# Kernel tuning notes

Hardware: AMD Instinct MI355X
Metric: run time of the kernel (lower is better)

## Reference

```python
import jax, jax.numpy as jnp
import numpy as np

B, T, D, H = 4, 2048, 1024, 16
HS = D // H  # 64
SCALE = float(HS) ** (-5)  # faithful to source: head_size ** (-5), NOT -0.5
EPS = 1e-5


def layer_norm(x, g, b):
    m = jnp.mean(x, axis=-1, keepdims=True)
    v = jnp.mean(jnp.square(x - m), axis=-1, keepdims=True)
    return (x - m) * jax.lax.rsqrt(v + EPS) * g + b


def setup_inputs() -> dict:
    key = jax.random.key(0)
    ks = jax.random.split(key, 8)
    s = 0.02
    return {
        "x": jax.random.normal(ks[0], (B, T, D), dtype=jnp.float32),
        "Wk": jax.random.normal(ks[1], (H, D, HS), dtype=jnp.float32) * s,  # shared by q (source bug: q = self.key(x))
        "Wv": jax.random.normal(ks[2], (H, D, HS), dtype=jnp.float32) * s,
        "Wo": jax.random.normal(ks[3], (H * HS, D), dtype=jnp.float32) * s,
        "bo": jnp.zeros((D,), dtype=jnp.float32),
        "g1": jnp.ones((D,), dtype=jnp.float32),
        "b1": jnp.zeros((D,), dtype=jnp.float32),
        "Wf1": jax.random.normal(ks[4], (D, D), dtype=jnp.float32) * s,
        "bf1": jnp.zeros((D,), dtype=jnp.float32),
        "Wf2": jax.random.normal(ks[5], (D, D), dtype=jnp.float32) * s,
        "bf2": jnp.zeros((D,), dtype=jnp.float32),
        "g2": jnp.ones((D,), dtype=jnp.float32),
        "b2": jnp.zeros((D,), dtype=jnp.float32),
    }


def reference(x, Wk, Wv, Wo, bo, g1, b1, Wf1, bf1, Wf2, bf2, g2, b2):
    # per-head projections; source uses key weights for BOTH q and k, so q == k
    k = jnp.einsum('btd,hds->bhts', x, Wk)           # [B,H,T,HS]
    v = jnp.einsum('btd,hds->bhts', x, Wv)           # [B,H,T,HS]
    wei = jnp.einsum('bhts,bhus->bhtu', k, k) * SCALE  # q==k; [B,H,T,T]
    causal = jnp.tril(jnp.ones((T, T), dtype=bool))
    wei = jnp.where(causal, wei, -jnp.inf)
    wei = jax.nn.softmax(wei, axis=-1)
    attn = jnp.einsum('bhtu,bhus->bhts', wei, v)     # [B,H,T,HS]
    cat = attn.transpose(0, 2, 1, 3).reshape(B, T, H * HS)  # concat heads
    attn_out = cat @ Wo + bo                         # output projection
    norm = layer_norm(attn_out + x, g1, b1)
    ff = jax.nn.relu(norm @ Wf1 + bf1) @ Wf2 + bf2
    return layer_norm(ff + norm + x, g2, b2)
```

## Files before the change

### kernel.cpp

```cpp
#include <hip/hip_runtime.h>

typedef unsigned short u16;
typedef __attribute__((ext_vector_type(8))) short short8;
typedef __attribute__((ext_vector_type(4))) float f32x4;

constexpr int Bn = 4, Tn = 2048, Dn = 1024, Hn = 16, HSn = 64;
constexpr long BT = (long)Bn * Tn;
#define NSEG 64
#define SEG (Tn / NSEG)

__device__ __forceinline__ u16 f2bf(float f) {
    union { float f; unsigned u; } x; x.f = f;
    unsigned r = x.u + 0x7FFFu + ((x.u >> 16) & 1u);
    return (u16)(r >> 16);
}
__device__ __forceinline__ float bf2f(unsigned bits16) {
    union { unsigned u; float f; } x; x.u = bits16 << 16;
    return x.f;
}

__device__ __forceinline__ void async_load16(const u16* g, u16* lds) {
    __builtin_amdgcn_global_load_lds(
        (const __attribute__((address_space(1))) unsigned*)g,
        (__attribute__((address_space(3))) unsigned*)lds, 16, 0, 0);
}

__global__ __launch_bounds__(256) void prep_kernel(
    const float* __restrict__ x, const float* __restrict__ Wv,
    const float* __restrict__ Wo, const float* __restrict__ Wf1,
    const float* __restrict__ Wf2,
    u16* __restrict__ xb, u16* __restrict__ WvC,
    u16* __restrict__ WoT, u16* __restrict__ Wf1T, u16* __restrict__ Wf2T)
{
    __shared__ float tile[32][33];
    const int blk = blockIdx.x;
    if (blk < 8192) {
        long i = (long)blk * 256 + threadIdx.x;
        float4 v = ((const float4*)x)[i];
        unsigned lo = (unsigned)f2bf(v.x) | ((unsigned)f2bf(v.y) << 16);
        unsigned hi = (unsigned)f2bf(v.z) | ((unsigned)f2bf(v.w) << 16);
        ((uint2*)xb)[i] = make_uint2(lo, hi);
    } else if (blk < 12288) {
        long i = (long)(blk - 8192) * 256 + threadIdx.x;
        int d = (int)(i >> 10), c = (int)(i & 1023);
        int h = c >> 6, s = c & 63;
        WvC[i] = f2bf(Wv[((long)h * Dn + d) * HSn + s]);
    } else {
        int idx = blk - 12288;
        int z = idx >> 10, rem = idx & 1023;
        const float* in = z == 0 ? Wo : (z == 1 ? Wf1 : Wf2);
        u16* out        = z == 0 ? WoT : (z == 1 ? Wf1T : Wf2T);
        int k0 = (rem & 31) * 32, n0 = (rem >> 5) * 32;
        int tx = threadIdx.x & 31, ty = threadIdx.x >> 5;
        #pragma unroll
        for (int r = 0; r < 4; r++)
            tile[ty + r * 8][tx] = in[(long)(k0 + ty + r * 8) * Dn + n0 + tx];
        __syncthreads();
        #pragma unroll
        for (int r = 0; r < 4; r++)
            out[(long)(n0 + ty + r * 8) * Dn + k0 + tx] = f2bf(tile[tx][ty + r * 8]);
    }
}

__global__ __launch_bounds__(256) void mfma_gemm(
    const u16* __restrict__ A,
    const u16* __restrict__ BT,
    float* __restrict__ Cf,
    u16* __restrict__ Cb,
    const float* __restrict__ bias, int relu, int K, int N,
    float* __restrict__ segs_out)
{
    __shared__ __attribute__((aligned(16))) u16 As[128 * 64];
    __shared__ __attribute__((aligned(16))) u16 Bs[128 * 64];

    const int t = threadIdx.x;
    const int wv = t >> 6, ln = t & 63;
    const int lane15 = ln & 15, q = ln >> 4;
    const int row0 = blockIdx.x * 128, n0 = blockIdx.y * 128;
    const int mq = (wv >> 1) * 64, nq = (wv & 1) * 64;

    f32x4 acc[4][4];
    #pragma unroll
    for (int i = 0; i < 4; i++)
        #pragma unroll
        for (int j = 0; j < 4; j++)
            acc[i][j] = (f32x4){0.f, 0.f, 0.f, 0.f};

    for (int k0 = 0; k0 < K; k0 += 64) {
        #pragma unroll
        for (int jj = 0; jj < 4; jj++) {
            int Ibase = wv * 256 + jj * 64;
            int I = Ibase + ln;
            int m = I >> 3, pc = I & 7, c = pc ^ (m & 7);
            async_load16(&A[(long)(row0 + m) * K + k0 + c * 8], &As[Ibase * 8]);
        }
        #pragma unroll
        for (int jj = 0; jj < 4; jj++) {
            int Ibase = wv * 256 + jj * 64;
            int I = Ibase + ln;
            int m = I >> 3, pc = I & 7, c = pc ^ (m & 7);
            async_load16(&BT[(long)(n0 + m) * K + k0 + c * 8], &Bs[Ibase * 8]);
        }
        __syncthreads();

        #pragma unroll
        for (int kk = 0; kk < 2; kk++) {
            short8 af[4], bfr[4];
            #pragma unroll
            for (int i = 0; i < 4; i++) {
                int mr = mq + i * 16 + lane15;
                int ca = (kk * 4 + q) ^ (mr & 7);
                af[i] = *(const short8*)&As[(mr * 8 + ca) * 8];
                int nr = nq + i * 16 + lane15;
                int cb = (kk * 4 + q) ^ (nr & 7);
                bfr[i] = *(const short8*)&Bs[(nr * 8 + cb) * 8];
            }
            #pragma unroll
            for (int i = 0; i < 4; i++)
                #pragma unroll
                for (int j = 0; j < 4; j++)
                    acc[i][j] = __builtin_amdgcn_mfma_f32_16x16x32_bf16(
                        af[i], bfr[j], acc[i][j], 0, 0, 0);
        }
        __syncthreads();
    }

    if (segs_out) {
        int segbase = (row0 + mq) >> 5;
        #pragma unroll
        for (int j = 0; j < 4; j++) {
            float s01 = 0.f, s23 = 0.f;
            #pragma unroll
            for (int r = 0; r < 4; r++) {
                s01 += acc[0][j][r] + acc[1][j][r];
                s23 += acc[2][j][r] + acc[3][j][r];
            }
            s01 += __shfl_xor(s01, 16); s01 += __shfl_xor(s01, 32);
            s23 += __shfl_xor(s23, 16); s23 += __shfl_xor(s23, 32);
            int col = n0 + nq + j * 16 + lane15;
            if (q == 0) segs_out[(long)segbase * Dn + col] = s01;
            if (q == 1) segs_out[(long)(segbase + 1) * Dn + col] = s23;
        }
    }

    #pragma unroll
    for (int j = 0; j < 4; j++) {
        int col = n0 + nq + j * 16 + lane15;
        float bv = bias ? bias[col] : 0.f;
        #pragma unroll
        for (int i = 0; i < 4; i++) {
            #pragma unroll
            for (int r = 0; r < 4; r++) {
                long row = row0 + mq + i * 16 + q * 4 + r;
                float v = acc[i][j][r] + bv;
                if (relu) v = fmaxf(v, 0.f);
                if (Cf) Cf[row * N + col] = v;
                if (Cb) Cb[row * N + col] = f2bf(v);
            }
        }
    }
}

__global__ __launch_bounds__(256) void mfma_gemm64(
    const u16* __restrict__ A, const u16* __restrict__ BT,
    u16* __restrict__ Cb, int K, int N)
{
    __shared__ __attribute__((aligned(16))) u16 As[64 * 64];
    __shared__ __attribute__((aligned(16))) u16 Bs[64 * 64];

    const int t = threadIdx.x;
    const int wv = t >> 6, ln = t & 63;
    const int lane15 = ln & 15, q = ln >> 4;
    const int row0 = blockIdx.x * 64, n0 = blockIdx.y * 64;
    const int mq = (wv >> 1) * 32, nq = (wv & 1) * 32;

    f32x4 acc[2][2];
    #pragma unroll
    for (int i = 0; i < 2; i++)
        #pragma unroll
        for (int j = 0; j < 2; j++)
            acc[i][j] = (f32x4){0.f, 0.f, 0.f, 0.f};

    for (int k0 = 0; k0 < K; k0 += 64) {
        #pragma unroll
        for (int jj = 0; jj < 2; jj++) {
            int Ibase = wv * 128 + jj * 64;
            int I = Ibase + ln;
            int m = I >> 3, pc = I & 7, c = pc ^ (m & 7);
            async_load16(&A[(long)(row0 + m) * K + k0 + c * 8], &As[Ibase * 8]);
        }
        #pragma unroll
        for (int jj = 0; jj < 2; jj++) {
            int Ibase = wv * 128 + jj * 64;
            int I = Ibase + ln;
            int m = I >> 3, pc = I & 7, c = pc ^ (m & 7);
            async_load16(&BT[(long)(n0 + m) * K + k0 + c * 8], &Bs[Ibase * 8]);
        }
        __syncthreads();

        #pragma unroll
        for (int kk = 0; kk < 2; kk++) {
            short8 af[2], bfr[2];
            #pragma unroll
            for (int i = 0; i < 2; i++) {
                int mr = mq + i * 16 + lane15;
                int ca = (kk * 4 + q) ^ (mr & 7);
                af[i] = *(const short8*)&As[(mr * 8 + ca) * 8];
                int nr = nq + i * 16 + lane15;
                int cb = (kk * 4 + q) ^ (nr & 7);
                bfr[i] = *(const short8*)&Bs[(nr * 8 + cb) * 8];
            }
            #pragma unroll
            for (int i = 0; i < 2; i++)
                #pragma unroll
                for (int j = 0; j < 2; j++)
                    acc[i][j] = __builtin_amdgcn_mfma_f32_16x16x32_bf16(
                        af[i], bfr[j], acc[i][j], 0, 0, 0);
        }
        __syncthreads();
    }

    #pragma unroll
    for (int j = 0; j < 2; j++) {
        int col = n0 + nq + j * 16 + lane15;
        #pragma unroll
        for (int i = 0; i < 2; i++)
            #pragma unroll
            for (int r = 0; r < 4; r++) {
                long row = row0 + mq + i * 16 + q * 4 + r;
                Cb[row * N + col] = f2bf(acc[i][j][r]);
            }
    }
}

__global__ __launch_bounds__(256) void scanln_kernel(
    const u16* __restrict__ y, const float* __restrict__ segs,
    const float* __restrict__ bo, const u16* __restrict__ xb,
    const float* __restrict__ g1, const float* __restrict__ b1,
    u16* __restrict__ nb)
{
    __shared__ float zs[16 * 1024];

    const int b = blockIdx.x, sg = blockIdx.y;
    const int t = threadIdx.x;
    const int lane = t & 63, w = t >> 6;

    float r0 = 0.f, r1 = 0.f, r2 = 0.f, r3 = 0.f;
    for (int s = 0; s < sg; s++) {
        float4 sv = ((const float4*)&segs[((long)(b * NSEG + s)) * Dn])[t];
        r0 += sv.x; r1 += sv.y; r2 += sv.z; r3 += sv.w;
    }
    const float4 bv = ((const float4*)bo)[t];

    float gv[16], be[16];
    #pragma unroll
    for (int j = 0; j < 4; j++) {
        *(float4*)&gv[j * 4] = *(const float4*)(g1 + j * 256 + lane * 4);
        *(float4*)&be[j * 4] = *(const float4*)(b1 + j * 256 + lane * 4);
    }

    const long rowu = ((long)b * Tn + (long)sg * SEG) * (Dn / 2);
    const unsigned* yu = (const unsigned*)y  + rowu;
    const unsigned* xu = (const unsigned*)xb + rowu;
    unsigned*       nu = (unsigned*)nb       + rowu;
    const int tb = sg * SEG;

    #pragma unroll
    for (int half = 0; half < 2; half++) {
        if (half) __syncthreads();
        for (int tt = 0; tt < 16; tt++) {
            int rowl = half * 16 + tt;
            uint2 uy = *(const uint2*)(yu + (long)rowl * 512 + 2 * t);
            r0 += bf2f(uy.x & 0xFFFFu); r1 += bf2f(uy.x >> 16);
            r2 += bf2f(uy.y & 0xFFFFu); r3 += bf2f(uy.y >> 16);
            uint2 ux = *(const uint2*)(xu + (long)rowl * 512 + 2 * t);
            float inv = 1.0f / (float)(tb + rowl + 1);
            float4 z4;
            z4.x = r0 * inv + bv.x + bf2f(ux.x & 0xFFFFu);
            z4.y = r1 * inv + bv.y + bf2f(ux.x >> 16);
            z4.z = r2 * inv + bv.z + bf2f(ux.y & 0xFFFFu);
            z4.w = r3 * inv + bv.w + bf2f(ux.y >> 16);
            *(float4*)&zs[tt * 1024 + 4 * t] = z4;
        }
        __syncthreads();
        #pragma unroll
        for (int k = 0; k < 4; k++) {
            int zrow = w * 4 + k;
            float f[16];
            #pragma unroll
            for (int j = 0; j < 4; j++)
                *(float4*)&f[j * 4] = *(const float4*)&zs[zrow * 1024 + j * 256 + lane * 4];
            float s = 0.f, ss = 0.f;
            #pragma unroll
            for (int i = 0; i < 16; i++) { s += f[i]; ss += f[i] * f[i]; }
            #pragma unroll
            for (int o = 1; o <= 32; o <<= 1) {
                s += __shfl_xor(s, o); ss += __shfl_xor(ss, o);
            }
            float mean = s * (1.0f / Dn);
            float var = ss * (1.0f / Dn) - mean * mean;
            float is = rsqrtf(var + 1e-5f);
            unsigned* op = nu + (long)(half * 16 + zrow) * 512;
            #pragma unroll
            for (int j = 0; j < 4; j++) {
                float e0 = (f[j * 4 + 0] - mean) * is * gv[j * 4 + 0] + be[j * 4 + 0];
                float e1 = (f[j * 4 + 1] - mean) * is * gv[j * 4 + 1] + be[j * 4 + 1];
                float e2 = (f[j * 4 + 2] - mean) * is * gv[j * 4 + 2] + be[j * 4 + 2];
                float e3 = (f[j * 4 + 3] - mean) * is * gv[j * 4 + 3] + be[j * 4 + 3];
                uint2 pk;
                pk.x = (unsigned)f2bf(e0) | ((unsigned)f2bf(e1) << 16);
                pk.y = (unsigned)f2bf(e2) | ((unsigned)f2bf(e3) << 16);
                *(uint2*)(op + j * 128 + 2 * lane) = pk;
            }
        }
    }
}

__global__ __launch_bounds__(256) void ln_kernel(
    const u16* __restrict__ a, const u16* __restrict__ b,
    const u16* __restrict__ c,
    const float* __restrict__ g, const float* __restrict__ beta,
    float* __restrict__ outf)
{
    const long base2 = (long)blockIdx.x * (Dn / 2);
    const int t = threadIdx.x;
    uint2 ua = ((const uint2*)((const unsigned*)a + base2))[t];
    float vx = bf2f(ua.x & 0xFFFFu), vy = bf2f(ua.x >> 16);
    float vz = bf2f(ua.y & 0xFFFFu), vw = bf2f(ua.y >> 16);
    uint2 ub = ((const uint2*)((const unsigned*)b + base2))[t];
    vx += bf2f(ub.x & 0xFFFFu); vy += bf2f(ub.x >> 16);
    vz += bf2f(ub.y & 0xFFFFu); vw += bf2f(ub.y >> 16);
    uint2 uc = ((const uint2*)((const unsigned*)c + base2))[t];
    vx += bf2f(uc.x & 0xFFFFu); vy += bf2f(uc.x >> 16);
    vz += bf2f(uc.y & 0xFFFFu); vw += bf2f(uc.y >> 16);

    __shared__ float sred[8];
    const int lane = t & 63, w = t >> 6;

    float s = vx + vy + vz + vw;
    #pragma unroll
    for (int o = 32; o > 0; o >>= 1) s += __shfl_down(s, o);
    if (lane == 0) sred[w] = s;
    __syncthreads();
    float mean = (sred[0] + sred[1] + sred[2] + sred[3]) * (1.0f / Dn);

    float dx = vx - mean, dy = vy - mean, dz = vz - mean, dw = vw - mean;
    float qq = dx * dx + dy * dy + dz * dz + dw * dw;
    #pragma unroll
    for (int o = 32; o > 0; o >>= 1) qq += __shfl_down(qq, o);
    if (lane == 0) sred[4 + w] = qq;
    __syncthreads();
    float var = (sred[4] + sred[5] + sred[6] + sred[7]) * (1.0f / Dn);
    float inv = rsqrtf(var + 1e-5f);

    float4 gg = ((const float4*)g)[t];
    float4 bb = ((const float4*)beta)[t];
    ((float4*)outf)[(long)blockIdx.x * 256 + t] = make_float4(
        dx * inv * gg.x + bb.x, dy * inv * gg.y + bb.y,
        dz * inv * gg.z + bb.z, dw * inv * gg.w + bb.w);
}

extern "C" void kernel_launch(void* const* d_in, const int* in_sizes, int n_in,
                              void* d_out, int out_size, void* d_ws, size_t ws_size,
                              hipStream_t stream) {
    const float* x   = (const float*)d_in[0];
    const float* Wv  = (const float*)d_in[2];
    const float* Wo  = (const float*)d_in[3];
    const float* bo  = (const float*)d_in[4];
    const float* g1  = (const float*)d_in[5];
    const float* b1  = (const float*)d_in[6];
    const float* Wf1 = (const float*)d_in[7];
    const float* bf1 = (const float*)d_in[8];
    const float* Wf2 = (const float*)d_in[9];
    const float* bf2 = (const float*)d_in[10];
    const float* g2  = (const float*)d_in[11];
    const float* b2  = (const float*)d_in[12];
    float* out = (float*)d_out;

    float* segs = (float*)d_ws;
    u16* xb   = (u16*)(segs + (long)Bn * NSEG * Dn);
    u16* yb   = xb + BT * Dn;
    u16* nb   = yb + BT * Dn;
    u16* fb   = nb + BT * Dn;
    u16* WoT  = fb + BT * Dn;
    u16* Wf1T = WoT + (long)Dn * Dn;
    u16* Wf2T = Wf1T + (long)Dn * Dn;
    u16* WvC  = Wf2T + (long)Dn * Dn;
    u16* WvoT = WvC + (long)Dn * Dn;

    dim3 blk(256);

    prep_kernel<<<dim3(15360), blk, 0, stream>>>(
        x, Wv, Wo, Wf1, Wf2, xb, WvC, WoT, Wf1T, Wf2T);

    mfma_gemm64<<<dim3(16, 16), blk, 0, stream>>>(WoT, WvC, WvoT, Dn, Dn);

    dim3 ggrid(BT / 128, Dn / 128);
    mfma_gemm<<<ggrid, blk, 0, stream>>>(
        xb, WvoT, nullptr, yb, nullptr, 0, Dn, Dn, segs);
    scanln_kernel<<<dim3(Bn, NSEG), blk, 0, stream>>>(
        yb, segs, bo, xb, g1, b1, nb);
    mfma_gemm<<<ggrid, blk, 0, stream>>>(
        nb, Wf1T, nullptr, fb, bf1, 1, Dn, Dn, nullptr);
    mfma_gemm<<<ggrid, blk, 0, stream>>>(
        fb, Wf2T, nullptr, yb, bf2, 0, Dn, Dn, nullptr);
    ln_kernel<<<dim3((unsigned)BT), blk, 0, stream>>>(
        yb, nb, xb, g2, b2, out);
}
```

Baseline: 144.8 us.

## Replace 128x128 GEMM with 256x128 triple-buffered async-pipelined 512-thread kernel

Measured after the change: 139.7 us, median of 2. -3.5%, faster.

```diff
diff --git a/kernel.cpp b/kernel.cpp
--- a/kernel.cpp
+++ b/kernel.cpp
@@ -62,100 +62,153 @@
     }
 }
 
-__global__ __launch_bounds__(256) void mfma_gemm(
+__device__ __forceinline__ void stageA256(const u16* __restrict__ Ag, u16* la,
+                                          int r, int wv, int ln, int row0,
+                                          int K, int kt) {
+    int Ib = r * 512 + wv * 64;
+    int I = Ib + ln;
+    int m = I >> 3, pc = I & 7, c = pc ^ (m & 7);
+    async_load16(&Ag[(long)(row0 + m) * K + kt * 64 + c * 8], &la[Ib * 8]);
+}
+__device__ __forceinline__ void stageB256(const u16* __restrict__ Bg, u16* lb,
+                                          int r, int wv, int ln, int n0,
+                                          int K, int kt) {
+    int Ib = r * 512 + wv * 64;
+    int I = Ib + ln;
+    int m = I >> 3, pc = I & 7, c = pc ^ (m & 7);
+    async_load16(&Bg[(long)(n0 + m) * K + kt * 64 + c * 8], &lb[Ib * 8]);
+}
+__device__ __forceinline__ short8 ldfrag(const u16* ls, int row, int lc) {
+    return *(const short8*)&ls[(row * 8 + (lc ^ (row & 7))) * 8];
+}
+
+__global__ __launch_bounds__(512) void mfma_gemm256(
     const u16* __restrict__ A,
-    const u16* __restrict__ BT,
-    float* __restrict__ Cf,
+    const u16* __restrict__ BTm,
     u16* __restrict__ Cb,
     const float* __restrict__ bias, int relu, int K, int N,
     float* __restrict__ segs_out)
 {
-    __shared__ __attribute__((aligned(16))) u16 As[128 * 64];
-    __shared__ __attribute__((aligned(16))) u16 Bs[128 * 64];
+    __shared__ __attribute__((aligned(16))) u16 As[3][256 * 64];
+    __shared__ __attribute__((aligned(16))) u16 Bs[3][128 * 64];
 
     const int t = threadIdx.x;
     const int wv = t >> 6, ln = t & 63;
-    const int lane15 = ln & 15, q = ln >> 4;
-    const int row0 = blockIdx.x * 128, n0 = blockIdx.y * 128;
-    const int mq = (wv >> 1) * 64, nq = (wv & 1) * 64;
-
-    f32x4 acc[4][4];
-    #pragma unroll
-    for (int i = 0; i < 4; i++)
-        #pragma unroll
-        for (int j = 0; j < 4; j++)
+    const int lane15 = ln & 15, qq = ln >> 4;
+    const int wr = wv >> 2, wc = wv & 3;
+    const int row0 = blockIdx.x * 256, n0 = blockIdx.y * 128;
+    const int NT = K >> 6;
+
+    f32x4 acc[8][2];
+    #pragma unroll
+    for (int i = 0; i < 8; i++)
+        #pragma unroll
+        for (int j = 0; j < 2; j++)
             acc[i][j] = (f32x4){0.f, 0.f, 0.f, 0.f};
 
-    for (int k0 = 0; k0 < K; k0 += 64) {
-        #pragma unroll
-        for (int jj = 0; jj < 4; jj++) {
-            int Ibase = wv * 256 + jj * 64;
-            int I = Ibase + ln;
-            int m = I >> 3, pc = I & 7, c = pc ^ (m & 7);
-            async_load16(&A[(long)(row0 + m) * K + k0 + c * 8], &As[Ibase * 8]);
-        }
-        #pragma unroll
-        for (int jj = 0; jj < 4; jj++) {
-            int Ibase = wv * 256 + jj * 64;
-            int I = Ibase + ln;
-            int m = I >> 3, pc = I & 7, c = pc ^ (m & 7);
-            async_load16(&BT[(long)(n0 + m) * K + k0 + c * 8], &Bs[Ibase * 8]);
-        }
-        __syncthreads();
-
-        #pragma unroll
-        for (int kk = 0; kk < 2; kk++) {
-            short8 af[4], bfr[4];
-            #pragma unroll
-            for (int i = 0; i < 4; i++) {
-                int mr = mq + i * 16 + lane15;
-                int ca = (kk * 4 + q) ^ (mr & 7);
-                af[i] = *(const short8*)&As[(mr * 8 + ca) * 8];
-                int nr = nq + i * 16 + lane15;
-                int cb = (kk * 4 + q) ^ (nr & 7);
-                bfr[i] = *(const short8*)&Bs[(nr * 8 + cb) * 8];
-            }
-            #pragma unroll
-            for (int i = 0; i < 4; i++)
+    u16 *A0 = &As[0][0], *A1 = &As[1][0], *A2 = &As[2][0];
+    u16 *B0 = &Bs[0][0], *B1 = &Bs[1][0], *B2 = &Bs[2][0];
+
+    #pragma unroll
+    for (int r = 0; r < 4; r++) stageA256(A, A0, r, wv, ln, row0, K, 0);
+    #pragma unroll
+    for (int r = 0; r < 2; r++) stageB256(BTm, B0, r, wv, ln, n0, K, 0);
+    #pragma unroll
+    for (int r = 0; r < 4; r++) stageA256(A, A1, r, wv, ln, row0, K, 1);
+    #pragma unroll
+    for (int r = 0; r < 2; r++) stageB256(BTm, B1, r, wv, ln, n0, K, 1);
+    asm volatile("s_waitcnt vmcnt(6)" ::: "memory");
+    __builtin_amdgcn_s_barrier();
+
+    for (int kt = 0; kt < NT; kt++) {
+        const bool st = (kt + 2 < NT);
+        short8 bq[2][2];
+        #pragma unroll
+        for (int ph = 0; ph < 4; ph++) {
+            short8 af[2][2];
+            #pragma unroll
+            for (int ii = 0; ii < 2; ii++) {
+                int ar = wr * 128 + (ph * 2 + ii) * 16 + lane15;
+                af[ii][0] = ldfrag(A0, ar, qq);
+                af[ii][1] = ldfrag(A0, ar, 4 + qq);
+            }
+            if (ph == 0) {
                 #pragma unroll
-                for (int j = 0; j < 4; j++)
-                    acc[i][j] = __builtin_amdgcn_mfma_f32_16x16x32_bf16(
-                        af[i], bfr[j], acc[i][j], 0, 0, 0);
-        }
-        __syncthreads();
+                for (int ng = 0; ng < 2; ng++) {
+                    int br = wc * 32 + ng * 16 + lane15;
+                    bq[ng][0] = ldfrag(B0, br, qq);
+                    bq[ng][1] = ldfrag(B0, br, 4 + qq);
+                }
+                if (st) {
+                    stageA256(A, A2, 0, wv, ln, row0, K, kt + 2);
+                    stageA256(A, A2, 1, wv, ln, row0, K, kt + 2);
+                }
+            } else if (ph == 1) {
+                if (st) {
+                    stageA256(A, A2, 2, wv, ln, row0, K, kt + 2);
+                    stageA256(A, A2, 3, wv, ln, row0, K, kt + 2);
+                }
+            } else if (ph == 2) {
+                if (st) {
+                    stageB256(BTm, B2, 0, wv, ln, n0, K, kt + 2);
+                    stageB256(BTm, B2, 1, wv, ln, n0, K, kt + 2);
+                }
+            }
+            __builtin_amdgcn_s_barrier();
+            __builtin_amdgcn_s_setprio(1);
+            #pragma unroll
+            for (int kk = 0; kk < 2; kk++)
+                #pragma unroll
+                for (int ii = 0; ii < 2; ii++)
+                    #pragma unroll
+                    for (int ng = 0; ng < 2; ng++)
+                        acc[ph * 2 + ii][ng] = __builtin_amdgcn_mfma_f32_16x16x32_bf16(
+                            af[ii][kk], bq[ng][kk], acc[ph * 2 + ii][ng], 0, 0, 0);
+            __builtin_amdgcn_s_setprio(0);
+            if (ph < 3) {
+                __builtin_amdgcn_s_barrier();
+            } else if (kt < NT - 1) {
+                if (st) asm volatile("s_waitcnt vmcnt(6)" ::: "memory");
+                else    asm volatile("s_waitcnt vmcnt(0)" ::: "memory");
+                __builtin_amdgcn_s_barrier();
+            }
+        }
+        u16* ta = A0; A0 = A1; A1 = A2; A2 = ta;
+        u16* tb = B0; B0 = B1; B1 = B2; B2 = tb;
     }
 
     if (segs_out) {
-        int segbase = (row0 + mq) >> 5;
-        #pragma unroll
-        for (int j = 0; j < 4; j++) {
-            float s01 = 0.f, s23 = 0.f;
+        int segbase = blockIdx.x * 8 + wr * 4;
+        #pragma unroll
+        for (int s = 0; s < 4; s++) {
+            #pragma unroll
+            for (int ng = 0; ng < 2; ng++) {
+                float sum = 0.f;
+                #pragma unroll
+                for (int r = 0; r < 4; r++)
+                    sum += acc[2 * s][ng][r] + acc[2 * s + 1][ng][r];
+                sum += __shfl_xor(sum, 16);
+                sum += __shfl_xor(sum, 32);
+                if (qq == 0) {
+                    int col = n0 + wc * 32 + ng * 16 + lane15;
+                    segs_out[(long)(segbase + s) * N + col] = sum;
+                }
+            }
+        }
+    }
+
+    #pragma unroll
+    for (int ng = 0; ng < 2; ng++) {
+        int col = n0 + wc * 32 + ng * 16 + lane15;
+        float bv = bias ? bias[col] : 0.f;
+        #pragma unroll
+        for (int i = 0; i < 8; i++) {
             #pragma unroll
             for (int r = 0; r < 4; r++) {
-                s01 += acc[0][j][r] + acc[1][j][r];
-                s23 += acc[2][j][r] + acc[3][j][r];
-            }
-            s01 += __shfl_xor(s01, 16); s01 += __shfl_xor(s01, 32);
-            s23 += __shfl_xor(s23, 16); s23 += __shfl_xor(s23, 32);
-            int col = n0 + nq + j * 16 + lane15;
-            if (q == 0) segs_out[(long)segbase * Dn + col] = s01;
-            if (q == 1) segs_out[(long)(segbase + 1) * Dn + col] = s23;
-        }
-    }
-
-    #pragma unroll
-    for (int j = 0; j < 4; j++) {
-        int col = n0 + nq + j * 16 + lane15;
-        float bv = bias ? bias[col] : 0.f;
-        #pragma unroll
-        for (int i = 0; i < 4; i++) {
-            #pragma unroll
-            for (int r = 0; r < 4; r++) {
-                long row = row0 + mq + i * 16 + q * 4 + r;
-                float v = acc[i][j][r] + bv;
+                long row = row0 + wr * 128 + i * 16 + qq * 4 + r;
+                float v = acc[i][ng][r] + bv;
                 if (relu) v = fmaxf(v, 0.f);
-                if (Cf) Cf[row * N + col] = v;
-                if (Cb) Cb[row * N + col] = f2bf(v);
+                Cb[row * N + col] = f2bf(v);
             }
         }
     }
@@ -395,15 +448,16 @@
 
     mfma_gemm64<<<dim3(16, 16), blk, 0, stream>>>(WoT, WvC, WvoT, Dn, Dn);
 
-    dim3 ggrid(BT / 128, Dn / 128);
-    mfma_gemm<<<ggrid, blk, 0, stream>>>(
-        xb, WvoT, nullptr, yb, nullptr, 0, Dn, Dn, segs);
+    dim3 ggrid(BT / 256, Dn / 128);
+    dim3 gblk(512);
+    mfma_gemm256<<<ggrid, gblk, 0, stream>>>(
+        xb, WvoT, yb, nullptr, 0, Dn, Dn, segs);
     scanln_kernel<<<dim3(Bn, NSEG), blk, 0, stream>>>(
         yb, segs, bo, xb, g1, b1, nb);
-    mfma_gemm<<<ggrid, blk, 0, stream>>>(
-        nb, Wf1T, nullptr, fb, bf1, 1, Dn, Dn, nullptr);
-    mfma_gemm<<<ggrid, blk, 0, stream>>>(
-        fb, Wf2T, nullptr, yb, bf2, 0, Dn, Dn, nullptr);
+    mfma_gemm256<<<ggrid, gblk, 0, stream>>>(
+        nb, Wf1T, fb, bf1, 1, Dn, Dn, nullptr);
+    mfma_gemm256<<<ggrid, gblk, 0, stream>>>(
+        fb, Wf2T, yb, bf2, 0, Dn, Dn, nullptr);
     ln_kernel<<<dim3((unsigned)BT), blk, 0, stream>>>(
         yb, nb, xb, g2, b2, out);
 }
```
